# Kernel optimization log

Hardware: AMD Instinct MI355X
Metric: run time of the kernel (lower is better)

## Reference

```python
import jax, jax.numpy as jnp
import numpy as np

EPS = 1e-5  # LayerNorm eps (torch default)
K_NN = 16   # matches init kwarg k


def _knn_idx(pos, k):
    # pos: (B,N,3) -> (B,N,k) indices of k nearest points (sorted by distance,
    # includes self at slot 0), matching pytorch3d knn_points(return_sorted=True).
    sq = jnp.sum(pos * pos, axis=-1)                                   # (B,N)
    d2 = sq[:, :, None] + sq[:, None, :] - 2.0 * jnp.einsum('bnd,bmd->bnm', pos, pos)
    _, idx = jax.lax.top_k(-d2, k)                                     # ascending distance
    return idx


def _gather(feats, idx):
    # feats: (B,N,C), idx: (B,N,K) -> (B,N,K,C)
    return jax.vmap(lambda f, i: f[i])(feats, idx)


def _ln(x, g, b):
    mu = jnp.mean(x, axis=-1, keepdims=True)
    var = jnp.mean((x - mu) ** 2, axis=-1, keepdims=True)
    return (x - mu) * jax.lax.rsqrt(var + EPS) * g + b


def setup_inputs() -> dict:
    key = jax.random.key(0)
    B, N, D, H = 2, 4096, 128, 12
    ks = jax.random.split(key, 16)
    s = 0.05
    f32 = jnp.float32
    return {
        'x': jax.random.normal(ks[0], (B, N, D), f32),
        'pos': jax.random.normal(ks[1], (B, N, 3), f32),
        # linear projections (bias=False)
        'w_q': jax.random.normal(ks[2], (D, D), f32) * s,
        'w_k': jax.random.normal(ks[3], (D, D), f32) * s,
        'w_v': jax.random.normal(ks[4], (D, D), f32) * s,
        # pos_mlp: Linear(3,H) -> LN(H) -> ReLU -> Linear(H,D)
        'pos_w1': jax.random.normal(ks[5], (H, 3), f32) * s,
        'pos_b1': jnp.zeros((H,), f32),
        'pos_g': jnp.ones((H,), f32),
        'pos_beta': jnp.zeros((H,), f32),
        'pos_w2': jax.random.normal(ks[6], (D, H), f32) * s,
        'pos_b2': jnp.zeros((D,), f32),
        # attn_mlp: Linear(D,D) -> LN(D) -> ReLU -> Linear(D,D)
        'attn_w1': jax.random.normal(ks[7], (D, D), f32) * s,
        'attn_b1': jnp.zeros((D,), f32),
        'attn_g': jnp.ones((D,), f32),
        'attn_beta': jnp.zeros((D,), f32),
        'attn_w2': jax.random.normal(ks[8], (D, D), f32) * s,
        'attn_b2': jnp.zeros((D,), f32),
    }


def reference(x, pos, w_q, w_k, w_v,
              pos_w1, pos_b1, pos_g, pos_beta, pos_w2, pos_b2,
              attn_w1, attn_b1, attn_g, attn_beta, attn_w2, attn_b2):
    idx = _knn_idx(pos, K_NN)                        # (B,N,K)
    q = x @ w_q.T                                    # (B,N,D)
    kf = _gather(x @ w_k.T, idx)                     # (B,N,K,D)
    vf = _gather(x @ w_v.T, idx)                     # (B,N,K,D)
    pos_rel = pos[:, :, None, :] - _gather(pos, idx)  # (B,N,K,3)
    # pos_mlp
    pe = _ln(pos_rel @ pos_w1.T + pos_b1, pos_g, pos_beta)
    pe = jax.nn.relu(pe) @ pos_w2.T + pos_b2         # (B,N,K,D)
    # attn_mlp on (q - k + pos_enc)
    w = q[:, :, None, :] - kf + pe
    w = _ln(w @ attn_w1.T + attn_b1, attn_g, attn_beta)
    w = jax.nn.relu(w) @ attn_w2.T + attn_b2         # (B,N,K,D)
    attn = jax.nn.softmax(w, axis=2)                 # softmax over neighbor dim
    return jnp.einsum('bnkd,bnkd->bnd', attn, vf + pe)
```

## Files before the change

### kernel.cpp

```cpp
#include <hip/hip_runtime.h>
#include <hip/hip_bf16.h>
#include <math.h>

#define BATCH 2
#define NPTS 4096
#define DIM 128
#define HID 12
#define KNN 16
#define NSLOT 24
#define BCAP 192
#define BCT 64

#define KNN_BLOCKS (BATCH * NPTS / 4)
#define FOLD_BLOCKS 128
#define PACK_BLOCKS 5

typedef __attribute__((ext_vector_type(8))) short short8;
typedef __attribute__((ext_vector_type(4))) float f32x4;

__device__ __forceinline__ short f2b(float f) {
  unsigned u = __float_as_uint(f);
  unsigned r = (u + 0x7fffu + ((u >> 16) & 1u)) >> 16;
  return (short)r;
}
__device__ __forceinline__ float b2f(short h) {
  return __uint_as_float(((unsigned)(unsigned short)h) << 16);
}

#define BITONIC64(v, vi)                                                     \
  {                                                                          \
    _Pragma("unroll") for (int k_ = 2; k_ <= 64; k_ <<= 1) {                 \
      _Pragma("unroll") for (int j_ = k_ >> 1; j_ >= 1; j_ >>= 1) {          \
        const float ov_ = __shfl_xor((v), j_);                               \
        const int oi_ = __shfl_xor((vi), j_);                                \
        const bool up_ = ((lane & k_) == 0);                                 \
        const bool lowpos_ = ((lane & j_) == 0);                             \
        const bool keep_min_ = (lowpos_ == up_);                             \
        const bool lt_ = (ov_ < (v)) || (ov_ == (v) && oi_ < (vi));          \
        const bool take_ = keep_min_ ? lt_ : !lt_;                           \
        if (take_) { (v) = ov_; (vi) = oi_; }                                \
      }                                                                      \
    }                                                                        \
  }

__device__ void knn_body(int bid, const float* __restrict__ pos,
                         int* __restrict__ knn_out) {
  __shared__ float bd_s[4][BCAP];
  __shared__ int bi_s[4][BCAP];

  const int t = threadIdx.x;
  const int w = t >> 6;
  const int lane = t & 63;
  const int n = (bid << 2) + w;
  const int b = n >> 12;
  const int qn = n & (NPTS - 1);

  float* bdl = &bd_s[w][0];
  int* bil = &bi_s[w][0];

  const float* pb = pos + b * NPTS * 3;
  const float qx = pb[qn * 3 + 0];
  const float qy = pb[qn * 3 + 1];
  const float qz = pb[qn * 3 + 2];

  const bool is_slot = (lane < NSLOT);
  float vald, thr;
  int validx;
  int bcount = 0;

  {
    const float2* pp = (const float2*)(pb + lane * 6);
    const float2 u0 = pp[0], u1 = pp[1], u2 = pp[2];
    float dx = qx - u0.x, dy = qy - u0.y, dz = qz - u1.x;
    float v = fmaf(dx, dx, fmaf(dy, dy, dz * dz));
    int vi = lane * 2;
    dx = qx - u1.y; dy = qy - u2.x; dz = qz - u2.y;
    const float d2b = fmaf(dx, dx, fmaf(dy, dy, dz * dz));

    BITONIC64(v, vi)
    vald = is_slot ? v : __builtin_inff();
    validx = is_slot ? vi : 0x7fffffff;
    const float v15 = __shfl(v, 15);
    thr = v15 + v15 * 1e-5f;

    const unsigned long long m = __ballot(d2b < thr);
    if (m) {
      const unsigned lt = __builtin_amdgcn_mbcnt_hi(
          (unsigned)(m >> 32), __builtin_amdgcn_mbcnt_lo((unsigned)m, 0u));
      if (d2b < thr) { bdl[lt] = d2b; bil[lt] = 2 * lane + 1; }
      bcount = (int)__builtin_popcountll(m);
    }
  }

  const float2* pp = (const float2*)(pb + 384 + lane * 6);
  float2 A0 = pp[0], A1 = pp[1], A2 = pp[2];
  pp = (const float2*)(pb + 768 + lane * 6);
  float2 B0 = pp[0], B1 = pp[1], B2 = pp[2];

#pragma unroll 1
  for (int it = 1; it < NPTS / 128; ++it) {
    const float2 c0 = A0, c1 = A1, c2 = A2;
    A0 = B0; A1 = B1; A2 = B2;
    if (it + 2 < NPTS / 128) {
      pp = (const float2*)(pb + (it + 2) * 384 + lane * 6);
      B0 = pp[0]; B1 = pp[1]; B2 = pp[2];
    }
    float dx = qx - c0.x, dy = qy - c0.y, dz = qz - c1.x;
    const float e2a = fmaf(dx, dx, fmaf(dy, dy, dz * dz));
    dx = qx - c1.y; dy = qy - c2.x; dz = qz - c2.y;
    const float e2b = fmaf(dx, dx, fmaf(dy, dy, dz * dz));

    if (bcount >= BCT) {
#pragma unroll 1
      while (bcount > 0) {
        const int take = bcount < 40 ? bcount : 40;
        float mv = __builtin_inff();
        int mi = 0x7fffffff;
        if (lane < NSLOT) { mv = vald; mi = validx; }
        else if (lane - NSLOT < take) {
          mv = bdl[bcount - take + lane - NSLOT];
          mi = bil[bcount - take + lane - NSLOT];
        }
        BITONIC64(mv, mi)
        if (is_slot) { vald = mv; validx = mi; }
        bcount -= take;
      }
      const float v15 = __shfl(vald, 15);
      thr = v15 + v15 * 1e-5f;
    }

    {
      const unsigned long long m = __ballot(e2a < thr);
      if (m) {
        const unsigned lt = __builtin_amdgcn_mbcnt_hi(
            (unsigned)(m >> 32), __builtin_amdgcn_mbcnt_lo((unsigned)m, 0u));
        if (e2a < thr) { bdl[bcount + lt] = e2a; bil[bcount + lt] = it * 128 + 2 * lane; }
        bcount += (int)__builtin_popcountll(m);
      }
    }
    {
      const unsigned long long m = __ballot(e2b < thr);
      if (m) {
        const unsigned lt = __builtin_amdgcn_mbcnt_hi(
            (unsigned)(m >> 32), __builtin_amdgcn_mbcnt_lo((unsigned)m, 0u));
        if (e2b < thr) { bdl[bcount + lt] = e2b; bil[bcount + lt] = it * 128 + 2 * lane + 1; }
        bcount += (int)__builtin_popcountll(m);
      }
    }
  }

#pragma unroll 1
  while (bcount > 0) {
    const int take = bcount < 40 ? bcount : 40;
    float mv = __builtin_inff();
    int mi = 0x7fffffff;
    if (lane < NSLOT) { mv = vald; mi = validx; }
    else if (lane - NSLOT < take) {
      mv = bdl[bcount - take + lane - NSLOT];
      mi = bil[bcount - take + lane - NSLOT];
    }
    BITONIC64(mv, mi)
    if (is_slot) { vald = mv; validx = mi; }
    bcount -= take;
  }

  double d2e = 1e300;
  if (is_slot) {
    const double ex = (double)qx - (double)pb[validx * 3 + 0];
    const double ey = (double)qy - (double)pb[validx * 3 + 1];
    const double ez = (double)qz - (double)pb[validx * 3 + 2];
    d2e = ex * ex + ey * ey + ez * ez;
  }
  int rank = 0;
#pragma unroll 1
  for (int j = 0; j < NSLOT; ++j) {
    const double dj = __shfl(d2e, j);
    const int ij = __shfl(validx, j);
    if (dj < d2e || (dj == d2e && ij < validx)) ++rank;
  }
  if (is_slot && rank < KNN) knn_out[((b << 12) + qn) * KNN + rank] = validx;
}

__device__ void fold_body(int bid, const float* __restrict__ aw1,
                          const float* __restrict__ wq, const float* __restrict__ wk,
                          short* __restrict__ WqaHi, short* __restrict__ WqaLo,
                          short* __restrict__ WkaHi, short* __restrict__ WkaLo) {
  const float* w = (bid < 64) ? wq : wk;
  short* oh = (bid < 64) ? WqaHi : WkaHi;
  short* ol = (bid < 64) ? WqaLo : WkaLo;
  const int row = ((bid & 63) << 1) + (threadIdx.x >> 7);
  const int i = threadIdx.x & 127;
  float acc = 0.f;
  for (int j = 0; j < 128; ++j) acc = fmaf(aw1[row * 128 + j], w[j * 128 + i], acc);
  const short h = f2b(acc);
  oh[row * 128 + i] = h;
  ol[row * 128 + i] = f2b(acc - b2f(h));
}

__device__ void pack_body(int bid, const float* __restrict__ aw1,
                          const float* __restrict__ pw2, const float* __restrict__ pb2,
                          const float* __restrict__ ab1, const float* __restrict__ aw2,
                          const float* __restrict__ wv,
                          short* __restrict__ M1b, short* __restrict__ pw2b,
                          short* __restrict__ aw2b, float* __restrict__ c1,
                          short* __restrict__ WvHi, short* __restrict__ WvLo) {
  const int t = threadIdx.x;
  if (bid == 0) {
    const int o = t >> 1, half = t & 1;
    for (int kk = 0; kk < 16; ++kk) {
      const int k = half * 16 + kk;
      float v = 0.f;
      if (k < HID)
        for (int j = 0; j < 128; ++j) v = fmaf(aw1[o * 128 + j], pw2[j * HID + k], v);
      M1b[o * 32 + k] = (k < HID) ? f2b(v) : (short)0;
    }
    if (t < 128) {
      float v = ab1[t];
      for (int j = 0; j < 128; ++j) v = fmaf(aw1[t * 128 + j], pb2[j], v);
      c1[t] = v;
    }
  } else if (bid == 1) {
    for (int i = t; i < 128 * 32; i += 256) {
      const int o = i >> 5, k = i & 31;
      pw2b[i] = (k < HID) ? f2b(pw2[o * HID + k]) : (short)0;
    }
  } else if (bid < 4) {
    const int base = (bid - 2) * 8192;
    for (int i = t; i < 8192; i += 256) aw2b[base + i] = f2b(aw2[base + i]);
  } else {
    for (int i = t; i < 128 * 128; i += 256) {
      const float v = wv[i];
      const short h = f2b(v);
      WvHi[i] = h;
      WvLo[i] = f2b(v - b2f(h));
    }
  }
}

__global__ __launch_bounds__(256) void knn_prep_kernel(
    const float* __restrict__ pos, int* __restrict__ knn_out,
    const float* __restrict__ aw1, const float* __restrict__ wq,
    const float* __restrict__ wk,
    short* __restrict__ WqaHi, short* __restrict__ WqaLo,
    short* __restrict__ WkaHi, short* __restrict__ WkaLo,
    const float* __restrict__ pw2, const float* __restrict__ pb2,
    const float* __restrict__ ab1, const float* __restrict__ aw2,
    const float* __restrict__ wv,
    short* __restrict__ M1b, short* __restrict__ pw2b, short* __restrict__ aw2b,
    float* __restrict__ c1, short* __restrict__ WvHi, short* __restrict__ WvLo) {
  const int bid = blockIdx.x;
  if (bid < KNN_BLOCKS) {
    knn_body(bid, pos, knn_out);
  } else if (bid < KNN_BLOCKS + FOLD_BLOCKS) {
    fold_body(bid - KNN_BLOCKS, aw1, wq, wk, WqaHi, WqaLo, WkaHi, WkaLo);
  } else {
    pack_body(bid - KNN_BLOCKS - FOLD_BLOCKS, aw1, pw2, pb2, ab1, aw2, wv, M1b,
              pw2b, aw2b, c1, WvHi, WvLo);
  }
}

__global__ __launch_bounds__(256) void proj_mfma_kernel(
    const float* __restrict__ x,
    const short* __restrict__ WqaHi, const short* __restrict__ WqaLo,
    const short* __restrict__ WkaHi, const short* __restrict__ WkaLo,
    const short* __restrict__ WvHi, const short* __restrict__ WvLo,
    float* __restrict__ QA, float* __restrict__ KA, float* __restrict__ Vp) {
  const int t = threadIdx.x;
  const int wid = t >> 6, lane = t & 63;
  const int r16 = lane & 15, g4 = lane >> 4;
  const int rowbase = blockIdx.x * 32 + (wid >> 1) * 16;
  const int ch = wid & 1;

  short8 ahi[4], alo[4];
#pragma unroll
  for (int ks = 0; ks < 4; ++ks) {
    const float* xp = x + (rowbase + r16) * DIM + ks * 32 + g4 * 8;
#pragma unroll
    for (int e = 0; e < 8; ++e) {
      const float v = xp[e];
      const short h = f2b(v);
      ahi[ks][e] = h;
      alo[ks][e] = f2b(v - b2f(h));
    }
  }

  const f32x4 zero4 = {0.f, 0.f, 0.f, 0.f};
  const short* WH[3] = {WqaHi, WkaHi, WvHi};
  const short* WL[3] = {WqaLo, WkaLo, WvLo};
  float* OUT[3] = {QA, KA, Vp};
#pragma unroll
  for (int mi = 0; mi < 3; ++mi) {
    const short* wh = WH[mi];
    const short* wl = WL[mi];
    float* o = OUT[mi];
#pragma unroll
    for (int q = 0; q < 4; ++q) {
      const int col = (ch * 4 + q) * 16 + r16;
      f32x4 a = zero4;
#pragma unroll
      for (int ks = 0; ks < 4; ++ks) {
        const short8 bh = *(const short8*)(wh + col * DIM + ks * 32 + g4 * 8);
        const short8 bl = *(const short8*)(wl + col * DIM + ks * 32 + g4 * 8);
        a = __builtin_amdgcn_mfma_f32_16x16x32_bf16(ahi[ks], bh, a, 0, 0, 0);
        a = __builtin_amdgcn_mfma_f32_16x16x32_bf16(alo[ks], bh, a, 0, 0, 0);
        a = __builtin_amdgcn_mfma_f32_16x16x32_bf16(ahi[ks], bl, a, 0, 0, 0);
      }
#pragma unroll
      for (int reg = 0; reg < 4; ++reg)
        o[(rowbase + g4 * 4 + reg) * DIM + (ch * 4 + q) * 16 + r16] = a[reg];
    }
  }
}

__global__ __launch_bounds__(256) void pt_wave_kernel(
    const float* __restrict__ pos, const int* __restrict__ knn_in,
    const float* __restrict__ QA, const float* __restrict__ KA, const float* __restrict__ Vp,
    const float* __restrict__ pw1, const float* __restrict__ pb1,
    const float* __restrict__ pg, const float* __restrict__ pbeta,
    const float* __restrict__ pb2,
    const float* __restrict__ ag, const float* __restrict__ abeta,
    const float* __restrict__ ab2, const float* __restrict__ c1,
    const short* __restrict__ M1b, const short* __restrict__ pw2b,
    const short* __restrict__ aw2b,
    float* __restrict__ out) {
  __shared__ __align__(16) short z_s[2048];
  __shared__ float red_s[2][4][16];

  const int t = threadIdx.x;
  const int wid = t >> 6;
  const int lane = t & 63;
  const int r16 = lane & 15;
  const int g4 = lane >> 4;
  const int n = blockIdx.x;
  const int b = n >> 12;

  const int jA = knn_in[n * KNN + r16];
  int jC[4];
#pragma unroll
  for (int reg = 0; reg < 4; ++reg) jC[reg] = knn_in[n * KNN + g4 * 4 + reg];

  const float qx = pos[n * 3 + 0], qy = pos[n * 3 + 1], qz = pos[n * 3 + 2];
  const int ja_g = b * NPTS + jA;
  const float rx = qx - pos[ja_g * 3 + 0];
  const float ry = qy - pos[ja_g * 3 + 1];
  const float rz = qz - pos[ja_g * 3 + 2];

  float hr[HID];
  {
    float mu = 0.f;
#pragma unroll
    for (int hh = 0; hh < HID; ++hh) {
      const float v = pb1[hh] + rx * pw1[hh * 3 + 0] + ry * pw1[hh * 3 + 1] +
                      rz * pw1[hh * 3 + 2];
      hr[hh] = v;
      mu += v;
    }
    mu *= (1.f / HID);
    float var = 0.f;
#pragma unroll
    for (int hh = 0; hh < HID; ++hh) { const float d = hr[hh] - mu; var = fmaf(d, d, var); }
    const float rs = rsqrtf(var * (1.f / HID) + 1e-5f);
#pragma unroll
    for (int hh = 0; hh < HID; ++hh)
      hr[hh] = fmaxf(fmaf((hr[hh] - mu) * rs, pg[hh], pbeta[hh]), 0.f);
  }

  short8 a1 = {0, 0, 0, 0, 0, 0, 0, 0};
  if (g4 == 0) {
#pragma unroll
    for (int e = 0; e < 8; ++e) a1[e] = f2b(hr[e]);
  } else if (g4 == 1) {
#pragma unroll
    for (int e = 0; e < 4; ++e) a1[e] = f2b(hr[8 + e]);
  }

  const f32x4 zero4 = {0.f, 0.f, 0.f, 0.f};
  f32x4 accw[2], accp[2];
#pragma unroll
  for (int q = 0; q < 2; ++q) {
    const int boff = ((wid * 2 + q) * 16 + r16) * 32 + g4 * 8;
    const short8 bm = *(const short8*)(M1b + boff);
    const short8 bp = *(const short8*)(pw2b + boff);
    accw[q] = __builtin_amdgcn_mfma_f32_16x16x32_bf16(a1, bm, zero4, 0, 0, 0);
    accp[q] = __builtin_amdgcn_mfma_f32_16x16x32_bf16(a1, bp, zero4, 0, 0, 0);
  }

  float w1v[2][4];
#pragma unroll
  for (int q = 0; q < 2; ++q) {
    const int o = (wid * 2 + q) * 16 + r16;
    const float base = QA[n * DIM + o] + c1[o];
#pragma unroll
    for (int reg = 0; reg < 4; ++reg) {
      const float ka = KA[(b * NPTS + jC[reg]) * DIM + o];
      w1v[q][reg] = accw[q][reg] + base - ka;
    }
  }

  {
    float ps[4], pq2[4];
#pragma unroll
    for (int reg = 0; reg < 4; ++reg) {
      ps[reg] = w1v[0][reg] + w1v[1][reg];
      pq2[reg] = fmaf(w1v[0][reg], w1v[0][reg], w1v[1][reg] * w1v[1][reg]);
    }
#pragma unroll
    for (int reg = 0; reg < 4; ++reg) {
#pragma unroll
      for (int off = 1; off <= 8; off <<= 1) {
        ps[reg] += __shfl_xor(ps[reg], off);
        pq2[reg] += __shfl_xor(pq2[reg], off);
      }
    }
    if (r16 == 0) {
#pragma unroll
      for (int reg = 0; reg < 4; ++reg) {
        red_s[0][wid][g4 * 4 + reg] = ps[reg];
        red_s[1][wid][g4 * 4 + reg] = pq2[reg];
      }
    }
  }
  __syncthreads();
  float mu[4], rs[4];
#pragma unroll
  for (int reg = 0; reg < 4; ++reg) {
    const int rr = g4 * 4 + reg;
    const float s = red_s[0][0][rr] + red_s[0][1][rr] + red_s[0][2][rr] + red_s[0][3][rr];
    const float q2 = red_s[1][0][rr] + red_s[1][1][rr] + red_s[1][2][rr] + red_s[1][3][rr];
    mu[reg] = s * (1.f / 128.f);
    const float var = q2 * (1.f / 128.f) - mu[reg] * mu[reg];
    rs[reg] = rsqrtf(var + 1e-5f);
  }

  {
    char* zb = (char*)z_s;
#pragma unroll
    for (int q = 0; q < 2; ++q) {
      const int o = (wid * 2 + q) * 16 + r16;
      const float gam = ag[o], bet = abeta[o];
#pragma unroll
      for (int reg = 0; reg < 4; ++reg) {
        const int rr = g4 * 4 + reg;
        const float zv = fmaxf(fmaf((w1v[q][reg] - mu[reg]) * rs[reg], gam, bet), 0.f);
        unsigned byte = (unsigned)(rr * 256 + o * 2);
        byte ^= ((unsigned)(rr & 7) << 4) ^ ((unsigned)(rr & 8) << 2);
        *(short*)(zb + byte) = f2b(zv);
      }
    }
  }
  __syncthreads();

  short8 a2[4];
  {
    const char* zb = (const char*)z_s;
#pragma unroll
    for (int ks = 0; ks < 4; ++ks) {
      unsigned byte = (unsigned)(r16 * 256 + ks * 64 + g4 * 16);
      byte ^= ((unsigned)(r16 & 7) << 4) ^ ((unsigned)(r16 & 8) << 2);
      a2[ks] = *(const short8*)(zb + byte);
    }
  }

  f32x4 acc2[2] = {zero4, zero4};
#pragma unroll
  for (int q = 0; q < 2; ++q) {
#pragma unroll
    for (int ks = 0; ks < 4; ++ks) {
      const short8 bw =
          *(const short8*)(aw2b + ((wid * 2 + q) * 16 + r16) * DIM + ks * 32 + g4 * 8);
      acc2[q] = __builtin_amdgcn_mfma_f32_16x16x32_bf16(a2[ks], bw, acc2[q], 0, 0, 0);
    }
  }

  float ew[2][4], inv[2];
#pragma unroll
  for (int q = 0; q < 2; ++q) {
    const float bb = ab2[(wid * 2 + q) * 16 + r16];
#pragma unroll
    for (int reg = 0; reg < 4; ++reg) ew[q][reg] = acc2[q][reg] + bb;
    float m = fmaxf(fmaxf(ew[q][0], ew[q][1]), fmaxf(ew[q][2], ew[q][3]));
    m = fmaxf(m, __shfl_xor(m, 16));
    m = fmaxf(m, __shfl_xor(m, 32));
    float s = 0.f;
#pragma unroll
    for (int reg = 0; reg < 4; ++reg) { ew[q][reg] = __expf(ew[q][reg] - m); s += ew[q][reg]; }
    s += __shfl_xor(s, 16);
    s += __shfl_xor(s, 32);
    inv[q] = 1.f / s;
  }

  float o_acc[2];
#pragma unroll
  for (int q = 0; q < 2; ++q) {
    const int o = (wid * 2 + q) * 16 + r16;
    const float pb = pb2[o];
    float acc = 0.f;
#pragma unroll
    for (int reg = 0; reg < 4; ++reg) {
      const float vv = Vp[(b * NPTS + jC[reg]) * DIM + o];
      acc = fmaf(ew[q][reg] * inv[q], vv + accp[q][reg] + pb, acc);
    }
    acc += __shfl_xor(acc, 16);
    acc += __shfl_xor(acc, 32);
    o_acc[q] = acc;
  }
  if (g4 < 2) out[n * DIM + (wid * 2 + g4) * 16 + r16] = o_acc[g4];
}

extern "C" void kernel_launch(void* const* d_in, const int* in_sizes, int n_in,
                              void* d_out, int out_size, void* d_ws, size_t ws_size,
                              hipStream_t stream) {
  const float* x   = (const float*)d_in[0];
  const float* pos = (const float*)d_in[1];
  const float* wq  = (const float*)d_in[2];
  const float* wk  = (const float*)d_in[3];
  const float* wv  = (const float*)d_in[4];
  const float* pw1 = (const float*)d_in[5];
  const float* pb1 = (const float*)d_in[6];
  const float* pg  = (const float*)d_in[7];
  const float* pbt = (const float*)d_in[8];
  const float* pw2 = (const float*)d_in[9];
  const float* pb2 = (const float*)d_in[10];
  const float* aw1 = (const float*)d_in[11];
  const float* ab1 = (const float*)d_in[12];
  const float* ag  = (const float*)d_in[13];
  const float* abt = (const float*)d_in[14];
  const float* aw2 = (const float*)d_in[15];
  const float* ab2 = (const float*)d_in[16];
  float* out = (float*)d_out;

  char* ws = (char*)d_ws;
  int*   knn   = (int*)ws;
  short* WqaHi = (short*)(ws + 512u * 1024u);
  short* WqaLo = (short*)(ws + 544u * 1024u);
  short* WkaHi = (short*)(ws + 576u * 1024u);
  short* WkaLo = (short*)(ws + 608u * 1024u);
  short* M1b   = (short*)(ws + 640u * 1024u);
  short* pw2b  = (short*)(ws + 648u * 1024u);
  short* aw2b  = (short*)(ws + 656u * 1024u);
  float* c1    = (float*)(ws + 688u * 1024u);
  short* WvHi  = (short*)(ws + 704u * 1024u);
  short* WvLo  = (short*)(ws + 736u * 1024u);
  float* QA    = (float*)(ws + (1u << 20));
  float* KA    = (float*)(ws + 5u * (1u << 20));
  float* Vp    = (float*)(ws + 9u * (1u << 20));

  knn_prep_kernel<<<KNN_BLOCKS + FOLD_BLOCKS + PACK_BLOCKS, 256, 0, stream>>>(
      pos, knn, aw1, wq, wk, WqaHi, WqaLo, WkaHi, WkaLo, pw2, pb2, ab1, aw2, wv,
      M1b, pw2b, aw2b, c1, WvHi, WvLo);
  proj_mfma_kernel<<<BATCH * NPTS / 32, 256, 0, stream>>>(
      x, WqaHi, WqaLo, WkaHi, WkaLo, WvHi, WvLo, QA, KA, Vp);
  pt_wave_kernel<<<BATCH * NPTS, 256, 0, stream>>>(
      pos, knn, QA, KA, Vp, pw1, pb1, pg, pbt, pb2, ag, abt, ab2, c1, M1b, pw2b, aw2b, out);
}
```

Measured before the change: 140.7 us.

## Schedule prep blocks first, parallelize M1 fold, and hoist neighbor loads

Prep work now runs in the first blocks of the fused kNN/prep launch, so the slow serial weight folds start early instead of trailing the kNN blocks. The single-block M1/c1 computation is split across 32 blocks using wave-wide shuffle reductions. In the attention kernel, the neighbor indices are loaded once and broadcast by shuffle. The Q/K/V gathers are issued up front so their latency overlaps the position-MLP math, at the cost of more live registers.

```diff
diff --git a/kernel.cpp b/kernel.cpp
--- a/kernel.cpp
+++ b/kernel.cpp
@@ -11,9 +11,10 @@
 #define BCAP 192
 #define BCT 64
 
+#define FOLD_BLOCKS 128
+#define M1_BLOCKS 32
+#define PRE_BLOCKS (FOLD_BLOCKS + M1_BLOCKS + 4)
 #define KNN_BLOCKS (BATCH * NPTS / 4)
-#define FOLD_BLOCKS 128
-#define PACK_BLOCKS 5
 
 typedef __attribute__((ext_vector_type(8))) short short8;
 typedef __attribute__((ext_vector_type(4))) float f32x4;
@@ -99,15 +100,15 @@
 
 #pragma unroll 1
   for (int it = 1; it < NPTS / 128; ++it) {
-    const float2 c0 = A0, c1 = A1, c2 = A2;
+    const float2 c0 = A0, c1v = A1, c2 = A2;
     A0 = B0; A1 = B1; A2 = B2;
     if (it + 2 < NPTS / 128) {
       pp = (const float2*)(pb + (it + 2) * 384 + lane * 6);
       B0 = pp[0]; B1 = pp[1]; B2 = pp[2];
     }
-    float dx = qx - c0.x, dy = qy - c0.y, dz = qz - c1.x;
+    float dx = qx - c0.x, dy = qy - c0.y, dz = qz - c1v.x;
     const float e2a = fmaf(dx, dx, fmaf(dy, dy, dz * dz));
-    dx = qx - c1.y; dy = qy - c2.x; dz = qz - c2.y;
+    dx = qx - c1v.y; dy = qy - c2.x; dz = qz - c2.y;
     const float e2b = fmaf(dx, dx, fmaf(dy, dy, dz * dz));
 
     if (bcount >= BCT) {
@@ -197,43 +198,50 @@
   ol[row * 128 + i] = f2b(acc - b2f(h));
 }
 
-__device__ void pack_body(int bid, const float* __restrict__ aw1,
-                          const float* __restrict__ pw2, const float* __restrict__ pb2,
-                          const float* __restrict__ ab1, const float* __restrict__ aw2,
-                          const float* __restrict__ wv,
-                          short* __restrict__ M1b, short* __restrict__ pw2b,
-                          short* __restrict__ aw2b, float* __restrict__ c1,
-                          short* __restrict__ WvHi, short* __restrict__ WvLo) {
+__device__ void m1_body(int bid, const float* __restrict__ aw1,
+                        const float* __restrict__ pw2, const float* __restrict__ pb2,
+                        const float* __restrict__ ab1,
+                        short* __restrict__ M1b, float* __restrict__ c1) {
   const int t = threadIdx.x;
-  if (bid == 0) {
-    const int o = t >> 1, half = t & 1;
-    for (int kk = 0; kk < 16; ++kk) {
-      const int k = half * 16 + kk;
-      float v = 0.f;
-      if (k < HID)
-        for (int j = 0; j < 128; ++j) v = fmaf(aw1[o * 128 + j], pw2[j * HID + k], v);
-      M1b[o * 32 + k] = (k < HID) ? f2b(v) : (short)0;
-    }
-    if (t < 128) {
-      float v = ab1[t];
-      for (int j = 0; j < 128; ++j) v = fmaf(aw1[t * 128 + j], pb2[j], v);
-      c1[t] = v;
-    }
-  } else if (bid == 1) {
-    for (int i = t; i < 128 * 32; i += 256) {
-      const int o = i >> 5, k = i & 31;
-      pw2b[i] = (k < HID) ? f2b(pw2[o * HID + k]) : (short)0;
-    }
-  } else if (bid < 4) {
-    const int base = (bid - 2) * 8192;
-    for (int i = t; i < 8192; i += 256) aw2b[base + i] = f2b(aw2[base + i]);
-  } else {
-    for (int i = t; i < 128 * 128; i += 256) {
-      const float v = wv[i];
-      const short h = f2b(v);
-      WvHi[i] = h;
-      WvLo[i] = f2b(v - b2f(h));
-    }
+  const int wid = t >> 6, lane = t & 63;
+  const int o = bid * 4 + wid;
+  const float a0 = aw1[o * 128 + lane];
+  const float a1 = aw1[o * 128 + 64 + lane];
+
+  float s = fmaf(a0, pb2[lane], a1 * pb2[64 + lane]);
+#pragma unroll
+  for (int off = 1; off < 64; off <<= 1) s += __shfl_xor(s, off);
+  if (lane == 0) c1[o] = ab1[o] + s;
+
+#pragma unroll
+  for (int k = 0; k < HID; ++k) {
+    float p = fmaf(a0, pw2[lane * HID + k], a1 * pw2[(64 + lane) * HID + k]);
+#pragma unroll
+    for (int off = 1; off < 64; off <<= 1) p += __shfl_xor(p, off);
+    if (lane == 0) M1b[o * 32 + k] = f2b(p);
+  }
+  if (lane >= HID && lane < 32) M1b[o * 32 + lane] = 0;
+}
+
+__device__ void pw2b_body(const float* __restrict__ pw2, short* __restrict__ pw2b) {
+  const int t = threadIdx.x;
+  for (int i = t; i < 128 * 32; i += 256) {
+    const int o = i >> 5, k = i & 31;
+    pw2b[i] = (k < HID) ? f2b(pw2[o * HID + k]) : (short)0;
+  }
+}
+__device__ void aw2b_body(int half, const float* __restrict__ aw2,
+                          short* __restrict__ aw2b) {
+  const int base = half * 8192;
+  for (int i = threadIdx.x; i < 8192; i += 256) aw2b[base + i] = f2b(aw2[base + i]);
+}
+__device__ void wv_body(const float* __restrict__ wv, short* __restrict__ WvHi,
+                        short* __restrict__ WvLo) {
+  for (int i = threadIdx.x; i < 128 * 128; i += 256) {
+    const float v = wv[i];
+    const short h = f2b(v);
+    WvHi[i] = h;
+    WvLo[i] = f2b(v - b2f(h));
   }
 }
 
@@ -249,13 +257,18 @@
     short* __restrict__ M1b, short* __restrict__ pw2b, short* __restrict__ aw2b,
     float* __restrict__ c1, short* __restrict__ WvHi, short* __restrict__ WvLo) {
   const int bid = blockIdx.x;
-  if (bid < KNN_BLOCKS) {
-    knn_body(bid, pos, knn_out);
-  } else if (bid < KNN_BLOCKS + FOLD_BLOCKS) {
-    fold_body(bid - KNN_BLOCKS, aw1, wq, wk, WqaHi, WqaLo, WkaHi, WkaLo);
+  if (bid < FOLD_BLOCKS) {
+    fold_body(bid, aw1, wq, wk, WqaHi, WqaLo, WkaHi, WkaLo);
+  } else if (bid < FOLD_BLOCKS + M1_BLOCKS) {
+    m1_body(bid - FOLD_BLOCKS, aw1, pw2, pb2, ab1, M1b, c1);
+  } else if (bid == FOLD_BLOCKS + M1_BLOCKS) {
+    pw2b_body(pw2, pw2b);
+  } else if (bid <= FOLD_BLOCKS + M1_BLOCKS + 2) {
+    aw2b_body(bid - (FOLD_BLOCKS + M1_BLOCKS + 1), aw2, aw2b);
+  } else if (bid == FOLD_BLOCKS + M1_BLOCKS + 3) {
+    wv_body(wv, WvHi, WvLo);
   } else {
-    pack_body(bid - KNN_BLOCKS - FOLD_BLOCKS, aw1, pw2, pb2, ab1, aw2, wv, M1b,
-              pw2b, aw2b, c1, WvHi, WvLo);
+    knn_body(bid - PRE_BLOCKS, pos, knn_out);
   }
 }
 
@@ -334,17 +347,33 @@
   const int n = blockIdx.x;
   const int b = n >> 12;
 
-  const int jA = knn_in[n * KNN + r16];
+  int myidx = 0;
+  if (lane < KNN) myidx = knn_in[n * KNN + lane];
+  const int jA = __shfl(myidx, r16);
   int jC[4];
 #pragma unroll
-  for (int reg = 0; reg < 4; ++reg) jC[reg] = knn_in[n * KNN + g4 * 4 + reg];
-
+  for (int reg = 0; reg < 4; ++reg) jC[reg] = __shfl(myidx, g4 * 4 + reg);
+
+  const int ja_g = b * NPTS + jA;
+  const float pjx = pos[ja_g * 3 + 0];
+  const float pjy = pos[ja_g * 3 + 1];
+  const float pjz = pos[ja_g * 3 + 2];
   const float qx = pos[n * 3 + 0], qy = pos[n * 3 + 1], qz = pos[n * 3 + 2];
-  const int ja_g = b * NPTS + jA;
-  const float rx = qx - pos[ja_g * 3 + 0];
-  const float ry = qy - pos[ja_g * 3 + 1];
-  const float rz = qz - pos[ja_g * 3 + 2];
-
+
+  float qa_[2], kav[2][4], vv[2][4];
+#pragma unroll
+  for (int q = 0; q < 2; ++q) {
+    const int o = (wid * 2 + q) * 16 + r16;
+    qa_[q] = QA[n * DIM + o];
+#pragma unroll
+    for (int reg = 0; reg < 4; ++reg) {
+      const int row = b * NPTS + jC[reg];
+      kav[q][reg] = KA[row * DIM + o];
+      vv[q][reg] = Vp[row * DIM + o];
+    }
+  }
+
+  const float rx = qx - pjx, ry = qy - pjy, rz = qz - pjz;
   float hr[HID];
   {
     float mu = 0.f;
@@ -389,12 +418,10 @@
 #pragma unroll
   for (int q = 0; q < 2; ++q) {
     const int o = (wid * 2 + q) * 16 + r16;
-    const float base = QA[n * DIM + o] + c1[o];
-#pragma unroll
-    for (int reg = 0; reg < 4; ++reg) {
-      const float ka = KA[(b * NPTS + jC[reg]) * DIM + o];
-      w1v[q][reg] = accw[q][reg] + base - ka;
-    }
+    const float base = qa_[q] + c1[o];
+#pragma unroll
+    for (int reg = 0; reg < 4; ++reg)
+      w1v[q][reg] = accw[q][reg] + base - kav[q][reg];
   }
 
   {
@@ -496,10 +523,8 @@
     const float pb = pb2[o];
     float acc = 0.f;
 #pragma unroll
-    for (int reg = 0; reg < 4; ++reg) {
-      const float vv = Vp[(b * NPTS + jC[reg]) * DIM + o];
-      acc = fmaf(ew[q][reg] * inv[q], vv + accp[q][reg] + pb, acc);
-    }
+    for (int reg = 0; reg < 4; ++reg)
+      acc = fmaf(ew[q][reg] * inv[q], vv[q][reg] + accp[q][reg] + pb, acc);
     acc += __shfl_xor(acc, 16);
     acc += __shfl_xor(acc, 32);
     o_acc[q] = acc;
@@ -545,7 +570,7 @@
   float* KA    = (float*)(ws + 5u * (1u << 20));
   float* Vp    = (float*)(ws + 9u * (1u << 20));
 
-  knn_prep_kernel<<<KNN_BLOCKS + FOLD_BLOCKS + PACK_BLOCKS, 256, 0, stream>>>(
+  knn_prep_kernel<<<PRE_BLOCKS + KNN_BLOCKS, 256, 0, stream>>>(
       pos, knn, aw1, wq, wk, WqaHi, WqaLo, WkaHi, WkaLo, pw2, pb2, ab1, aw2, wv,
       M1b, pw2b, aw2b, c1, WvHi, WvLo);
   proj_mfma_kernel<<<BATCH * NPTS / 32, 256, 0, stream>>>(
```

Result: faster. 121.9 us (-13.3%).
